# Kernel optimization log

Measured on AMD Instinct MI355X. Metric: run time of the kernel, lower is better.

Reference implementation:

```python
import jax, jax.numpy as jnp
import numpy as np

N = 12000   # atoms per side
K = 32      # neighbors per point per radius
E = N * K   # edges per radius
R = 1500    # residues per side
P = 4096    # correspondence pairs
LN_EPS = 1e-5


def setup_inputs() -> dict:
    rng = np.random.default_rng(0)

    def unit(v):
        return (v / np.linalg.norm(v, axis=-1, keepdims=True)).astype(np.float32)

    pos_A = (rng.standard_normal((N, 3)) * 10.0).astype(np.float32)
    pos_B = (rng.standard_normal((N, 3)) * 10.0).astype(np.float32)
    normal_A = unit(rng.standard_normal((N, 3)))
    normal_B = unit(rng.standard_normal((N, 3)))

    def make_edges():
        dst = np.repeat(np.arange(N), K)                      # every node is a target
        src = (dst + 1 + rng.integers(0, N - 1, size=dst.shape)) % N  # src != dst
        return np.stack([src, dst]).astype(np.int32)          # [2, E]

    edges_A = np.stack([make_edges() for _ in range(3)])      # [3, 2, E]
    edges_B = np.stack([make_edges() for _ in range(3)])

    residue_idx_A = (np.arange(N) // (N // R)).astype(np.int32)
    residue_idx_B = (np.arange(N) // (N // R)).astype(np.int32)
    src_idx = rng.integers(0, R, P).astype(np.int32)
    tgt_idx = rng.integers(0, R, P).astype(np.int32)

    g = lambda *s: (rng.standard_normal(s) * 0.2).astype(np.float32)
    inp = dict(
        pos_A=jnp.asarray(pos_A), normal_A=jnp.asarray(normal_A),
        pos_B=jnp.asarray(pos_B), normal_B=jnp.asarray(normal_B),
        edges_A=jnp.asarray(edges_A), edges_B=jnp.asarray(edges_B),
        residue_idx_A=jnp.asarray(residue_idx_A), residue_idx_B=jnp.asarray(residue_idx_B),
        src_idx=jnp.asarray(src_idx), tgt_idx=jnp.asarray(tgt_idx),
        num_res=R,
        conv_w1=jnp.asarray(g(3, 4, 4)), conv_b1=jnp.zeros((3, 4), jnp.float32),
        conv_g1=jnp.ones((3, 4), jnp.float32), conv_be1=jnp.zeros((3, 4), jnp.float32),
        conv_w2=jnp.asarray(g(3, 4, 128)), conv_b2=jnp.zeros((3, 128), jnp.float32),
        conv_g2=jnp.ones((3, 128), jnp.float32), conv_be2=jnp.zeros((3, 128), jnp.float32),
        atom_w=jnp.asarray(g(384, 512)) * 0.25, atom_b=jnp.zeros((512,), jnp.float32),
        atom_g=jnp.ones((512,), jnp.float32), atom_be=jnp.zeros((512,), jnp.float32),
        res_w=jnp.asarray(g(512, 512)) * 0.25, res_b=jnp.zeros((512,), jnp.float32),
        res_g=jnp.ones((512,), jnp.float32), res_be=jnp.zeros((512,), jnp.float32),
        lin1_w=jnp.asarray(g(512, 1)), lin1_b=jnp.zeros((1,), jnp.float32),
    )
    return inp


def _mlp_layer(x, w, b, g, be):
    # Seq(Linear, ReLU, LayerNorm, Dropout(eval)) from MLP()
    h = jax.nn.relu(x @ w + b)
    mu = jnp.mean(h, axis=-1, keepdims=True)
    var = jnp.mean((h - mu) ** 2, axis=-1, keepdims=True)
    return g * (h - mu) * jax.lax.rsqrt(var + LN_EPS) + be


def _angle(v1, v2):
    c = jnp.cross(v1, v2)
    return jnp.arctan2(jnp.linalg.norm(c, axis=-1), jnp.sum(v1 * v2, axis=-1))


def _ppf(pos, normal, src, dst):
    # PyG point_pair_features: [||d||, <(n_i,d), <(n_j,d), <(n_i,n_j)], d = pos_j - pos_i
    d = pos[src] - pos[dst]
    dist = jnp.linalg.norm(d, axis=-1)
    n_i, n_j = normal[dst], normal[src]
    return jnp.stack([dist, _angle(n_i, d), _angle(n_j, d), _angle(n_i, n_j)], axis=-1)  # [E,4]


def reference(pos_A, normal_A, pos_B, normal_B, edges_A, edges_B,
              residue_idx_A, residue_idx_B, src_idx, tgt_idx, num_res,
              conv_w1, conv_b1, conv_g1, conv_be1, conv_w2, conv_b2, conv_g2, conv_be2,
              atom_w, atom_b, atom_g, atom_be, res_w, res_b, res_g, res_be,
              lin1_w, lin1_b):
    n = pos_A.shape[0]

    def side(pos, normal, edges):
        feats = []
        for r in range(3):  # conv2, conv3, conv4 (shared across A/B sides)
            src, dst = edges[r, 0], edges[r, 1]
            f = _ppf(pos, normal, src, dst)                         # [E,4]
            h = _mlp_layer(f, conv_w1[r], conv_b1[r], conv_g1[r], conv_be1[r])
            h = _mlp_layer(h, conv_w2[r], conv_b2[r], conv_g2[r], conv_be2[r])  # [E,128]
            feats.append(jax.ops.segment_max(h, dst, num_segments=n))          # [N,128]
        x = jnp.concatenate(feats, axis=-1)                         # [N,384]
        return _mlp_layer(x, atom_w, atom_b, atom_g, atom_be)       # [N,512]

    atom_x_A = side(pos_A, normal_A, edges_A)
    atom_x_B = side(pos_B, normal_B, edges_B)

    res_x_A = jax.ops.segment_max(atom_x_A, residue_idx_A, num_segments=num_res)
    res_x_B = jax.ops.segment_max(atom_x_B, residue_idx_B, num_segments=num_res)
    res_x_A = _mlp_layer(res_x_A, res_w, res_b, res_g, res_be)
    res_x_B = _mlp_layer(res_x_B, res_w, res_b, res_g, res_be)

    x_s = res_x_A[src_idx]
    x_t = res_x_B[tgt_idx]
    out = (x_s - x_t) @ lin1_w + lin1_b                              # [P,1]
    return jax.nn.sigmoid(out)
```

## Files before the change

### kernel.cpp

```cpp
#include <hip/hip_runtime.h>
#include <hip/hip_bf16.h>
#include <math.h>

#define N_ATOMS 12000
#define K_NB 32
#define E_EDGES (N_ATOMS*K_NB)
#define R_RES 1500
#define P_PAIRS 4096
#define LN_EPS 1e-5f

typedef __attribute__((ext_vector_type(8))) short short8;
typedef __attribute__((ext_vector_type(4))) float f32x4;
typedef __attribute__((ext_vector_type(4))) unsigned int u32x4;

__device__ __forceinline__ f32x4 splat4(float v){ f32x4 r = {v,v,v,v}; return r; }

__device__ __forceinline__ unsigned short f2bf(float f){
  unsigned u = __builtin_bit_cast(unsigned, f);
  u += 0x7FFF + ((u >> 16) & 1);
  return (unsigned short)(u >> 16);
}

template<int CTRL>
__device__ __forceinline__ float dpp_add(float v){
  int x = __builtin_amdgcn_mov_dpp(__builtin_bit_cast(int, v), CTRL, 0xf, 0xf, true);
  return v + __builtin_bit_cast(float, x);
}
__device__ __forceinline__ float dpp16sum(float v){
  v = dpp_add<0xB1>(v);
  v = dpp_add<0x4E>(v);
  v = dpp_add<0x141>(v);
  v = dpp_add<0x140>(v);
  return v;
}

__device__ __forceinline__ float fast_atan2(float y, float x){
  float ax = fabsf(x);
  float mn = fminf(ax, y);
  float mx = fmaxf(fmaxf(ax, y), 1e-30f);
  float r  = __builtin_amdgcn_rcpf(mx);
  r = r * (2.0f - mx * r);
  float a = mn * r;
  float s = a * a;
  float p = -0.0117212f;
  p = fmaf(p, s,  0.05265332f);
  p = fmaf(p, s, -0.11643287f);
  p = fmaf(p, s,  0.19354346f);
  p = fmaf(p, s, -0.33262347f);
  p = fmaf(p, s,  0.99997726f);
  p = p * a;
  p = (y > ax) ? (1.57079632679f - p) : p;
  p = (x < 0.f) ? (3.14159265359f - p) : p;
  return p;
}

__device__ __forceinline__ float angle3(float ax,float ay,float az,
                                        float bx,float by,float bz){
  float cx = ay*bz - az*by;
  float cy = az*bx - ax*bz;
  float cz = ax*by - ay*bx;
  float cn = sqrtf(cx*cx + cy*cy + cz*cz);
  float dt = ax*bx + ay*by + az*bz;
  return fast_atan2(cn, dt);
}

__global__ __launch_bounds__(256) void wpack_kernel(
    const float* __restrict__ w, unsigned short* __restrict__ wp, int Kdim)
{
  int idx = blockIdx.x*256 + threadIdx.x;
  if (idx >= Kdim*512) return;
  int k = idx >> 9, n = idx & 511;
  wp[(size_t)(k>>5)*512*32 + n*32 + (k&31)] = f2bf(w[idx]);
}

__global__ __launch_bounds__(256) void edge_fused_kernel(
    const float* __restrict__ pos_A, const float* __restrict__ nrm_A,
    const float* __restrict__ pos_B, const float* __restrict__ nrm_B,
    const int* __restrict__ edges_A, const int* __restrict__ edges_B,
    const float* __restrict__ w1, const float* __restrict__ b1,
    const float* __restrict__ g1, const float* __restrict__ be1,
    const float* __restrict__ w2, const float* __restrict__ b2,
    const float* __restrict__ g2, const float* __restrict__ be2,
    unsigned short* __restrict__ feats_A, unsigned short* __restrict__ feats_B)
{
  const int r = blockIdx.y;
  const int side = blockIdx.z;
  const float* __restrict__ pos = side ? pos_B : pos_A;
  const float* __restrict__ nrm = side ? nrm_B : nrm_A;
  const int* __restrict__ edges = (side ? edges_B : edges_A) + r*(2*E_EDGES);
  unsigned short* __restrict__ feats = side ? feats_B : feats_A;

  const int tid  = threadIdx.x;
  const int wv   = tid >> 6;
  const int lane = tid & 63;
  const int l15  = lane & 15;
  const bool live = (lane < 16);

  const float* __restrict__ w1r  = w1  + r*16;
  const float* __restrict__ b1r  = b1  + r*4;
  const float* __restrict__ g1r  = g1  + r*4;
  const float* __restrict__ be1r = be1 + r*4;
  const float* __restrict__ w2r  = w2  + r*512;

  short8 bfrag[8];
  float bias[8], gg[8], ee[8];
  #pragma unroll
  for (int ct = 0; ct < 8; ++ct) {
    int n = ct*16 + l15;
    float v0 = w2r[0*128+n], v1 = w2r[1*128+n];
    float v2 = w2r[2*128+n], v3 = w2r[3*128+n];
    short8 bf = {0,0,0,0,0,0,0,0};
    bf[0] = live ? (short)f2bf(v0) : (short)0;
    bf[1] = live ? (short)f2bf(v1) : (short)0;
    bf[2] = live ? (short)f2bf(v2) : (short)0;
    bf[3] = live ? (short)f2bf(v3) : (short)0;
    bfrag[ct] = bf;
    bias[ct] = b2[r*128+n];
    gg[ct]   = g2[r*128+n];
    ee[ct]   = be2[r*128+n];
  }

  const int node0 = blockIdx.x*32 + wv*8;
  const f32x4 zero4 = splat4(0.f);

  for (int win = 0; win < 4; ++win) {
    const int e = (node0 + win*2)*K_NB + lane;
    const int src = edges[e];
    const int dst = e >> 5;

    float psx = pos[src*3+0], psy = pos[src*3+1], psz = pos[src*3+2];
    float pdx = pos[dst*3+0], pdy = pos[dst*3+1], pdz = pos[dst*3+2];
    float dx = psx-pdx, dy = psy-pdy, dz = psz-pdz;
    float nix = nrm[dst*3+0], niy = nrm[dst*3+1], niz = nrm[dst*3+2];
    float njx = nrm[src*3+0], njy = nrm[src*3+1], njz = nrm[src*3+2];

    float f0 = sqrtf(dx*dx + dy*dy + dz*dz);
    float f1 = angle3(nix,niy,niz, dx,dy,dz);
    float f2 = angle3(njx,njy,njz, dx,dy,dz);
    float f3 = angle3(nix,niy,niz, njx,njy,njz);

    float h[4]; float s1 = 0.f;
    #pragma unroll
    for (int j = 0; j < 4; ++j) {
      float t = b1r[j] + f0*w1r[j] + f1*w1r[4+j] + f2*w1r[8+j] + f3*w1r[12+j];
      t = fmaxf(t, 0.f);
      h[j] = t; s1 += t;
    }
    float mu1 = s1*0.25f;
    float v1 = 0.f;
    #pragma unroll
    for (int j = 0; j < 4; ++j) { float d = h[j]-mu1; v1 += d*d; }
    float inv1 = rsqrtf(v1*0.25f + LN_EPS);
    float a0 = g1r[0]*(h[0]-mu1)*inv1 + be1r[0];
    float a1 = g1r[1]*(h[1]-mu1)*inv1 + be1r[1];
    float a2 = g1r[2]*(h[2]-mu1)*inv1 + be1r[2];
    float a3 = g1r[3]*(h[3]-mu1)*inv1 + be1r[3];

    unsigned alo = (unsigned)f2bf(a0) | ((unsigned)f2bf(a1) << 16);
    unsigned ahi = (unsigned)f2bf(a2) | ((unsigned)f2bf(a3) << 16);

    #pragma unroll
    for (int nd2 = 0; nd2 < 2; ++nd2) {
      float nodemax[8];
      #pragma unroll
      for (int ct = 0; ct < 8; ++ct) nodemax[ct] = -3.4e38f;

      #pragma unroll
      for (int rt = 0; rt < 2; ++rt) {
        const int srcl = nd2*32 + rt*16 + l15;
        unsigned palo = __shfl(alo, srcl, 64);
        unsigned pahi = __shfl(ahi, srcl, 64);
        palo = live ? palo : 0u;
        pahi = live ? pahi : 0u;
        u32x4 pk = {palo, pahi, 0u, 0u};
        short8 af = __builtin_bit_cast(short8, pk);

        f32x4 acc[8];
        #pragma unroll
        for (int ct = 0; ct < 8; ++ct)
          acc[ct] = __builtin_amdgcn_mfma_f32_16x16x32_bf16(af, bfrag[ct], zero4, 0, 0, 0);

        float p[4] = {0,0,0,0}, q[4] = {0,0,0,0};
        #pragma unroll
        for (int ct = 0; ct < 8; ++ct) {
          #pragma unroll
          for (int i = 0; i < 4; ++i) {
            float t = fmaxf(acc[ct][i] + bias[ct], 0.f);
            acc[ct][i] = t; p[i] += t; q[i] = fmaf(t, t, q[i]);
          }
        }
        #pragma unroll
        for (int i = 0; i < 4; ++i) {
          p[i] = dpp16sum(p[i]);
          q[i] = dpp16sum(q[i]);
        }
        float uu[4], vv[4];
        #pragma unroll
        for (int i = 0; i < 4; ++i) {
          float mu  = p[i]*(1.f/128.f);
          float var = fmaxf(q[i]*(1.f/128.f) - mu*mu, 0.f);
          float inv = rsqrtf(var + LN_EPS);
          uu[i] = inv; vv[i] = -mu*inv;
        }
        #pragma unroll
        for (int ct = 0; ct < 8; ++ct) {
          float vm = -3.4e38f;
          #pragma unroll
          for (int i = 0; i < 4; ++i) {
            float val = gg[ct]*fmaf(acc[ct][i], uu[i], vv[i]) + ee[ct];
            vm = fmaxf(vm, val);
          }
          nodemax[ct] = fmaxf(nodemax[ct], vm);
        }
      }

      #pragma unroll
      for (int ct = 0; ct < 8; ++ct) {
        float vm = nodemax[ct];
        vm = fmaxf(vm, __shfl_xor(vm, 16, 64));
        vm = fmaxf(vm, __shfl_xor(vm, 32, 64));
        nodemax[ct] = vm;
      }

      if (live) {
        const int gnode = node0 + win*2 + nd2;
        #pragma unroll
        for (int ct = 0; ct < 8; ++ct)
          feats[(size_t)gnode*384 + r*128 + ct*16 + l15] = f2bf(nodemax[ct]);
      }
    }
  }
}

__global__ __launch_bounds__(256) void gemm_ln_kernel(
    const unsigned short* __restrict__ x_A, const unsigned short* __restrict__ x_B,
    const unsigned short* __restrict__ wp,
    const float* __restrict__ b, const float* __restrict__ g,
    const float* __restrict__ be,
    float* __restrict__ out_A, float* __restrict__ out_B,
    int nrows, int Kdim)
{
  const unsigned short* __restrict__ x = blockIdx.y ? x_B : x_A;
  float* __restrict__ out = blockIdx.y ? out_B : out_A;

  __shared__ __align__(16) unsigned short sA[64*40];
  __shared__ __align__(16) unsigned short sB[512*40];
  __shared__ float sb[512], sg[512], sbe[512];

  const int tid  = threadIdx.x;
  const int wv   = tid >> 6;
  const int lane = tid & 63;
  const int l15  = lane & 15;
  const int quad = lane >> 4;
  const int rbase = blockIdx.x * 64;

  sb[tid]      = b[tid];    sb[tid+256]  = b[tid+256];
  sg[tid]      = g[tid];    sg[tid+256]  = g[tid+256];
  sbe[tid]     = be[tid];   sbe[tid+256] = be[tid+256];

  const f32x4 zero4 = splat4(0.f);
  f32x4 acc[32];
  #pragma unroll
  for (int ct = 0; ct < 32; ++ct) acc[ct] = zero4;

  const int nchunk = Kdim >> 5;
  const int arow = tid >> 2, apart = tid & 3;
  int agr = rbase + arow; if (agr >= nrows) agr = nrows - 1;
  const unsigned short* aptr = x + (size_t)agr*Kdim + apart*8;

  for (int kc = 0; kc < nchunk; ++kc) {
    __syncthreads();
    *(float4*)&sA[arow*40 + apart*8] = *(const float4*)(aptr + kc*32);
    {
      const float4* src = (const float4*)(wp + (size_t)kc*512*32);
      #pragma unroll
      for (int i = 0; i < 8; ++i) {
        int fi = tid + i*256;
        int n = fi >> 2, part = fi & 3;
        *(float4*)&sB[n*40 + part*8] = src[fi];
      }
    }
    __syncthreads();
    short8 af = *(short8*)&sA[(wv*16 + l15)*40 + quad*8];
    #pragma unroll
    for (int ct = 0; ct < 32; ++ct) {
      short8 bf = *(short8*)&sB[(ct*16 + l15)*40 + quad*8];
      acc[ct] = __builtin_amdgcn_mfma_f32_16x16x32_bf16(af, bf, acc[ct], 0, 0, 0);
    }
  }

  f32x4 p = zero4, q = zero4;
  #pragma unroll
  for (int ct = 0; ct < 32; ++ct) {
    f32x4 t = __builtin_elementwise_max(acc[ct] + splat4(sb[ct*16 + l15]), zero4);
    acc[ct] = t;
    p += t;
    q += t * t;
  }
  #pragma unroll
  for (int i = 0; i < 4; ++i) {
    p[i] = dpp16sum(p[i]);
    q[i] = dpp16sum(q[i]);
  }
  f32x4 mu4  = p * splat4(1.f/512.f);
  f32x4 var4 = __builtin_elementwise_max(q * splat4(1.f/512.f) - mu4*mu4, zero4);
  f32x4 uu, vv;
  #pragma unroll
  for (int i = 0; i < 4; ++i) {
    float inv = rsqrtf(var4[i] + LN_EPS);
    uu[i] = inv; vv[i] = -mu4[i]*inv;
  }
  const int row0 = rbase + wv*16 + quad*4;
  #pragma unroll
  for (int ct = 0; ct < 32; ++ct) {
    int gcol = ct*16 + l15;
    f32x4 v = acc[ct]*uu + vv;
    v = splat4(sg[gcol])*v + splat4(sbe[gcol]);
    #pragma unroll
    for (int i = 0; i < 4; ++i) {
      int grow = row0 + i;
      if (grow < nrows)
        out[(size_t)grow*512 + gcol] = v[i];
    }
  }
}

__global__ __launch_bounds__(256) void gemm_ln_res_kernel(
    const float* __restrict__ ax_A, const float* __restrict__ ax_B,
    const unsigned short* __restrict__ wp,
    const float* __restrict__ b, const float* __restrict__ g,
    const float* __restrict__ be,
    float* __restrict__ out_A, float* __restrict__ out_B)
{
  const float* __restrict__ ax = blockIdx.y ? ax_B : ax_A;
  float* __restrict__ out = blockIdx.y ? out_B : out_A;

  __shared__ __align__(16) unsigned short sA[64*40];
  __shared__ __align__(16) unsigned short sB[512*40];
  __shared__ float sb[512], sg[512], sbe[512];

  const int tid  = threadIdx.x;
  const int wv   = tid >> 6;
  const int lane = tid & 63;
  const int l15  = lane & 15;
  const int quad = lane >> 4;
  const int rbase = blockIdx.x * 64;

  sb[tid]      = b[tid];    sb[tid+256]  = b[tid+256];
  sg[tid]      = g[tid];    sg[tid+256]  = g[tid+256];
  sbe[tid]     = be[tid];   sbe[tid+256] = be[tid+256];

  const f32x4 zero4 = splat4(0.f);
  f32x4 acc[32];
  #pragma unroll
  for (int ct = 0; ct < 32; ++ct) acc[ct] = zero4;

  const int arow = tid >> 2, apart = tid & 3;
  int rres = rbase + arow; if (rres >= R_RES) rres = R_RES - 1;
  const float* abase = ax + (size_t)rres*8*512 + apart*8;

  for (int kc = 0; kc < 16; ++kc) {
    __syncthreads();
    {
      const float* ap = abase + kc*32;
      float4 m0 = *(const float4*)(ap);
      float4 m1 = *(const float4*)(ap + 4);
      #pragma unroll
      for (int a = 1; a < 8; ++a) {
        float4 v0 = *(const float4*)(ap + (size_t)a*512);
        float4 v1 = *(const float4*)(ap + (size_t)a*512 + 4);
        m0.x = fmaxf(m0.x, v0.x); m0.y = fmaxf(m0.y, v0.y);
        m0.z = fmaxf(m0.z, v0.z); m0.w = fmaxf(m0.w, v0.w);
        m1.x = fmaxf(m1.x, v1.x); m1.y = fmaxf(m1.y, v1.y);
        m1.z = fmaxf(m1.z, v1.z); m1.w = fmaxf(m1.w, v1.w);
      }
      ushort4 o0, o1;
      o0.x = f2bf(m0.x); o0.y = f2bf(m0.y); o0.z = f2bf(m0.z); o0.w = f2bf(m0.w);
      o1.x = f2bf(m1.x); o1.y = f2bf(m1.y); o1.z = f2bf(m1.z); o1.w = f2bf(m1.w);
      *(ushort4*)&sA[arow*40 + apart*8]     = o0;
      *(ushort4*)&sA[arow*40 + apart*8 + 4] = o1;
    }
    {
      const float4* src = (const float4*)(wp + (size_t)kc*512*32);
      #pragma unroll
      for (int i = 0; i < 8; ++i) {
        int fi = tid + i*256;
        int n = fi >> 2, part = fi & 3;
        *(float4*)&sB[n*40 + part*8] = src[fi];
      }
    }
    __syncthreads();
    short8 af = *(short8*)&sA[(wv*16 + l15)*40 + quad*8];
    #pragma unroll
    for (int ct = 0; ct < 32; ++ct) {
      short8 bf = *(short8*)&sB[(ct*16 + l15)*40 + quad*8];
      acc[ct] = __builtin_amdgcn_mfma_f32_16x16x32_bf16(af, bf, acc[ct], 0, 0, 0);
    }
  }

  f32x4 p = zero4, q = zero4;
  #pragma unroll
  for (int ct = 0; ct < 32; ++ct) {
    f32x4 t = __builtin_elementwise_max(acc[ct] + splat4(sb[ct*16 + l15]), zero4);
    acc[ct] = t;
    p += t;
    q += t * t;
  }
  #pragma unroll
  for (int i = 0; i < 4; ++i) {
    p[i] = dpp16sum(p[i]);
    q[i] = dpp16sum(q[i]);
  }
  f32x4 mu4  = p * splat4(1.f/512.f);
  f32x4 var4 = __builtin_elementwise_max(q * splat4(1.f/512.f) - mu4*mu4, zero4);
  f32x4 uu, vv;
  #pragma unroll
  for (int i = 0; i < 4; ++i) {
    float inv = rsqrtf(var4[i] + LN_EPS);
    uu[i] = inv; vv[i] = -mu4[i]*inv;
  }
  const int row0 = rbase + wv*16 + quad*4;
  #pragma unroll
  for (int ct = 0; ct < 32; ++ct) {
    int gcol = ct*16 + l15;
    f32x4 v = acc[ct]*uu + vv;
    v = splat4(sg[gcol])*v + splat4(sbe[gcol]);
    #pragma unroll
    for (int i = 0; i < 4; ++i) {
      int grow = row0 + i;
      if (grow < R_RES)
        out[(size_t)grow*512 + gcol] = v[i];
    }
  }
}

__global__ __launch_bounds__(256) void final_kernel(
    const float* __restrict__ resx_A, const float* __restrict__ resx_B,
    const int* __restrict__ src_idx, const int* __restrict__ tgt_idx,
    const float* __restrict__ lin_w, const float* __restrict__ lin_b,
    float* __restrict__ outp)
{
  int idx = blockIdx.x*256 + threadIdx.x;
  int p  = idx >> 3;
  int l8 = idx & 7;
  if (p >= P_PAIRS) return;
  const float4* xa = (const float4*)(resx_A + (size_t)src_idx[p]*512) + l8;
  const float4* xb = (const float4*)(resx_B + (size_t)tgt_idx[p]*512) + l8;
  const float4* wv = (const float4*)lin_w + l8;
  float acc = 0.f;
  #pragma unroll
  for (int i = 0; i < 16; ++i) {
    float4 a = xa[i*8], b = xb[i*8], w = wv[i*8];
    acc += (a.x-b.x)*w.x + (a.y-b.y)*w.y + (a.z-b.z)*w.z + (a.w-b.w)*w.w;
  }
  acc += __shfl_xor(acc, 1, 64);
  acc += __shfl_xor(acc, 2, 64);
  acc += __shfl_xor(acc, 4, 64);
  if (l8 == 0) {
    acc += lin_b[0];
    outp[p] = 1.f/(1.f + expf(-acc));
  }
}

extern "C" void kernel_launch(void* const* d_in, const int* in_sizes, int n_in,
                              void* d_out, int out_size, void* d_ws, size_t ws_size,
                              hipStream_t stream)
{
  const float* pos_A   = (const float*)d_in[0];
  const float* nrm_A   = (const float*)d_in[1];
  const float* pos_B   = (const float*)d_in[2];
  const float* nrm_B   = (const float*)d_in[3];
  const int*   edges_A = (const int*)d_in[4];
  const int*   edges_B = (const int*)d_in[5];
  const int*   src_idx = (const int*)d_in[8];
  const int*   tgt_idx = (const int*)d_in[9];
  const float* conv_w1  = (const float*)d_in[11];
  const float* conv_b1  = (const float*)d_in[12];
  const float* conv_g1  = (const float*)d_in[13];
  const float* conv_be1 = (const float*)d_in[14];
  const float* conv_w2  = (const float*)d_in[15];
  const float* conv_b2  = (const float*)d_in[16];
  const float* conv_g2  = (const float*)d_in[17];
  const float* conv_be2 = (const float*)d_in[18];
  const float* atom_w   = (const float*)d_in[19];
  const float* atom_b   = (const float*)d_in[20];
  const float* atom_g   = (const float*)d_in[21];
  const float* atom_be  = (const float*)d_in[22];
  const float* res_w    = (const float*)d_in[23];
  const float* res_b    = (const float*)d_in[24];
  const float* res_g    = (const float*)d_in[25];
  const float* res_be   = (const float*)d_in[26];
  const float* lin1_w   = (const float*)d_in[27];
  const float* lin1_b   = (const float*)d_in[28];

  unsigned short* feats_A = (unsigned short*)d_ws;
  unsigned short* feats_B = feats_A + (size_t)N_ATOMS*384;
  float* atomx_A = (float*)(feats_B + (size_t)N_ATOMS*384);
  float* atomx_B = atomx_A + (size_t)N_ATOMS*512;
  float* resx_A  = atomx_B + (size_t)N_ATOMS*512;
  float* resx_B  = resx_A + (size_t)R_RES*512;
  unsigned short* wpA = (unsigned short*)(resx_B + (size_t)R_RES*512);
  unsigned short* wpB = wpA + (size_t)384*512;

  wpack_kernel<<<(384*512)/256, 256, 0, stream>>>(atom_w, wpA, 384);
  wpack_kernel<<<(512*512)/256, 256, 0, stream>>>(res_w, wpB, 512);

  dim3 gG(N_ATOMS/32, 3, 2);
  edge_fused_kernel<<<gG, 256, 0, stream>>>(pos_A, nrm_A, pos_B, nrm_B,
      edges_A, edges_B,
      conv_w1, conv_b1, conv_g1, conv_be1,
      conv_w2, conv_b2, conv_g2, conv_be2,
      feats_A, feats_B);

  dim3 gAtom((N_ATOMS + 63)/64, 2);
  gemm_ln_kernel<<<gAtom, 256, 0, stream>>>(feats_A, feats_B, wpA,
      atom_b, atom_g, atom_be, atomx_A, atomx_B, N_ATOMS, 384);

  dim3 gRes((R_RES + 63)/64, 2);
  gemm_ln_res_kernel<<<gRes, 256, 0, stream>>>(atomx_A, atomx_B, wpB,
      res_b, res_g, res_be, resx_A, resx_B);

  final_kernel<<<(P_PAIRS*8 + 255)/256, 256, 0, stream>>>(resx_A, resx_B,
      src_idx, tgt_idx, lin1_w, lin1_b, (float*)d_out);
}
```

Measured before the change: 324.0 us.

## Load GEMM weight tiles directly to LDS with XOR-swizzled packed layout

The weight tile staging in both GEMM+LayerNorm kernels now uses global_load_lds (direct global-to-LDS 16-byte loads) instead of going through registers. Padding is replaced by an XOR swizzle of the 16-byte groups, applied in the weight packing kernel and mirrored in the LDS read address. This is meant to cut VGPR traffic and LDS footprint in the weight loads while keeping bank conflicts low. It relies on the direct-to-LDS builtin's per-wave contiguous placement semantics being correct.

```diff
diff --git a/kernel.cpp b/kernel.cpp
--- a/kernel.cpp
+++ b/kernel.cpp
@@ -19,6 +19,12 @@
   unsigned u = __builtin_bit_cast(unsigned, f);
   u += 0x7FFF + ((u >> 16) & 1);
   return (unsigned short)(u >> 16);
+}
+
+__device__ __forceinline__ void load_lds_16B(const void* gsrc, void* lds_dst){
+  __builtin_amdgcn_global_load_lds(
+      (const __attribute__((address_space(1))) unsigned int*)gsrc,
+      (__attribute__((address_space(3))) unsigned int*)lds_dst, 16, 0, 0);
 }
 
 template<int CTRL>
@@ -70,7 +76,10 @@
   int idx = blockIdx.x*256 + threadIdx.x;
   if (idx >= Kdim*512) return;
   int k = idx >> 9, n = idx & 511;
-  wp[(size_t)(k>>5)*512*32 + n*32 + (k&31)] = f2bf(w[idx]);
+  int kc = k >> 5, kin = k & 31;
+  int quad = kin >> 3, j = kin & 7;
+  int g = n*4 + (quad ^ ((n>>2)&3));
+  wp[(size_t)kc*16384 + g*8 + j] = f2bf(w[idx]);
 }
 
 __global__ __launch_bounds__(256) void edge_fused_kernel(
@@ -244,7 +253,7 @@
   float* __restrict__ out = blockIdx.y ? out_B : out_A;
 
   __shared__ __align__(16) unsigned short sA[64*40];
-  __shared__ __align__(16) unsigned short sB[512*40];
+  __shared__ __align__(16) unsigned short sB[512*32];
   __shared__ float sb[512], sg[512], sbe[512];
 
   const int tid  = threadIdx.x;
@@ -272,19 +281,20 @@
     __syncthreads();
     *(float4*)&sA[arow*40 + apart*8] = *(const float4*)(aptr + kc*32);
     {
-      const float4* src = (const float4*)(wp + (size_t)kc*512*32);
+      const unsigned short* wsrc = wp + (size_t)kc*16384;
       #pragma unroll
       for (int i = 0; i < 8; ++i) {
-        int fi = tid + i*256;
-        int n = fi >> 2, part = fi & 3;
-        *(float4*)&sB[n*40 + part*8] = src[fi];
+        int g0 = (wv*8 + i)*64;
+        load_lds_16B(wsrc + (size_t)(g0 + lane)*8, &sB[g0*8]);
       }
     }
     __syncthreads();
     short8 af = *(short8*)&sA[(wv*16 + l15)*40 + quad*8];
     #pragma unroll
     for (int ct = 0; ct < 32; ++ct) {
-      short8 bf = *(short8*)&sB[(ct*16 + l15)*40 + quad*8];
+      int n = ct*16 + l15;
+      int gidx = n*4 + (quad ^ ((n>>2)&3));
+      short8 bf = *(short8*)&sB[gidx*8];
       acc[ct] = __builtin_amdgcn_mfma_f32_16x16x32_bf16(af, bf, acc[ct], 0, 0, 0);
     }
   }
@@ -336,7 +346,7 @@
   float* __restrict__ out = blockIdx.y ? out_B : out_A;
 
   __shared__ __align__(16) unsigned short sA[64*40];
-  __shared__ __align__(16) unsigned short sB[512*40];
+  __shared__ __align__(16) unsigned short sB[512*32];
   __shared__ float sb[512], sg[512], sbe[512];
 
   const int tid  = threadIdx.x;
@@ -381,19 +391,20 @@
       *(ushort4*)&sA[arow*40 + apart*8 + 4] = o1;
     }
     {
-      const float4* src = (const float4*)(wp + (size_t)kc*512*32);
+      const unsigned short* wsrc = wp + (size_t)kc*16384;
       #pragma unroll
       for (int i = 0; i < 8; ++i) {
-        int fi = tid + i*256;
-        int n = fi >> 2, part = fi & 3;
-        *(float4*)&sB[n*40 + part*8] = src[fi];
+        int g0 = (wv*8 + i)*64;
+        load_lds_16B(wsrc + (size_t)(g0 + lane)*8, &sB[g0*8]);
       }
     }
     __syncthreads();
     short8 af = *(short8*)&sA[(wv*16 + l15)*40 + quad*8];
     #pragma unroll
     for (int ct = 0; ct < 32; ++ct) {
-      short8 bf = *(short8*)&sB[(ct*16 + l15)*40 + quad*8];
+      int n = ct*16 + l15;
+      int gidx = n*4 + (quad ^ ((n>>2)&3));
+      short8 bf = *(short8*)&sB[gidx*8];
       acc[ct] = __builtin_amdgcn_mfma_f32_16x16x32_bf16(af, bf, acc[ct], 0, 0, 0);
     }
   }
```

Measured after the change: 319.2 us. No clear change (-1.5%).
